# Kernel optimization log

Hardware: AMD Instinct MI355X
Metric: run time of the kernel (lower is better)

## Reference

```python
import jax, jax.numpy as jnp
import numpy as np

MODEL_DIM = 1024
NUM_HEADS = 16
HEAD_DIM = MODEL_DIM // NUM_HEADS
ROPE_THETA = 10000.0


def _rotate_half(x):
    x1, x2 = jnp.split(x, 2, axis=-1)
    return jnp.concatenate((-x2, x1), axis=-1)


def _rope_cos_sin(seq_len, dtype):
    inv_freq = 1.0 / (ROPE_THETA ** (jnp.arange(0, HEAD_DIM, 2, dtype=jnp.float32) / HEAD_DIM))
    pos = jnp.arange(seq_len, dtype=jnp.float32)
    freqs = jnp.einsum('i,j->ij', pos, inv_freq)  # [S, HEAD_DIM/2]
    emb = jnp.concatenate((freqs, freqs), axis=-1)  # [S, HEAD_DIM]
    return jnp.cos(emb).astype(dtype), jnp.sin(emb).astype(dtype)


def setup_inputs() -> dict:
    key = jax.random.key(0)
    ks = jax.random.split(key, 9)
    B, S, D = 4, 2048, MODEL_DIM
    scale = 1.0 / np.sqrt(D)
    inp = {
        'x': jax.random.normal(ks[0], (B, S, D), dtype=jnp.float32),
        'key_padding_mask': jnp.ones((B, S), dtype=bool),
        'wq': jax.random.normal(ks[1], (D, D), dtype=jnp.float32) * scale,
        'bq': jnp.zeros((D,), dtype=jnp.float32),
        'wk': jax.random.normal(ks[2], (D, D), dtype=jnp.float32) * scale,
        'bk': jnp.zeros((D,), dtype=jnp.float32),
        'wv': jax.random.normal(ks[3], (D, D), dtype=jnp.float32) * scale,
        'bv': jnp.zeros((D,), dtype=jnp.float32),
        'wo': jax.random.normal(ks[4], (D, D), dtype=jnp.float32) * scale,
        'bo': jnp.zeros((D,), dtype=jnp.float32),
    }
    return inp


def reference(x, key_padding_mask, wq, bq, wk, bk, wv, bv, wo, bo):
    B, S, D = x.shape
    H, Hd = NUM_HEADS, HEAD_DIM
    q = (x @ wq + bq).reshape(B, S, H, Hd).transpose(0, 2, 1, 3)
    k = (x @ wk + bk).reshape(B, S, H, Hd).transpose(0, 2, 1, 3)
    v = (x @ wv + bv).reshape(B, S, H, Hd).transpose(0, 2, 1, 3)
    cos, sin = _rope_cos_sin(S, x.dtype)  # [S, Hd]
    cos = cos[None, None]
    sin = sin[None, None]
    q = q * cos + _rotate_half(q) * sin
    k = k * cos + _rotate_half(k) * sin
    scores = jnp.einsum('bhqd,bhkd->bhqk', q, k) / jnp.sqrt(jnp.asarray(Hd, x.dtype))
    mask = key_padding_mask[:, None, None, :]
    scores = jnp.where(mask, scores, jnp.finfo(scores.dtype).min)
    attn = jax.nn.softmax(scores, axis=-1)
    ctx = jnp.einsum('bhqk,bhkd->bhqd', attn, v)
    ctx = ctx.transpose(0, 2, 1, 3).reshape(B, S, D)
    out = ctx @ wo + bo
    out = out * key_padding_mask[:, :, None].astype(out.dtype)
    return out
```

## Files before the change

### kernel.cpp

```cpp
#include <hip/hip_runtime.h>
#include <math.h>

#define S_LEN  2048
#define NH     16
#define HD     64
#define DMODEL 1024
#define BATCH  4
#define M_TOK  (BATCH * S_LEN)

typedef __bf16 bf16x8 __attribute__((ext_vector_type(8)));
typedef float  floatx4 __attribute__((ext_vector_type(4)));
typedef float  floatx16 __attribute__((ext_vector_type(16)));

typedef __attribute__((address_space(1))) const void cg_void;
typedef __attribute__((address_space(3))) void lds_void;

__device__ __forceinline__ void gload16(const void* g, void* l) {
    __builtin_amdgcn_global_load_lds((cg_void*)g, (lds_void*)l, 16, 0, 0);
}

__device__ __forceinline__ unsigned short f2bf(float f) {
    unsigned int u = __builtin_bit_cast(unsigned int, f);
    u = (u + 0x7FFF + ((u >> 16) & 1)) >> 16;
    return (unsigned short)u;
}

__device__ __forceinline__ unsigned cvtpk(float lo, float hi) {
    unsigned r;
    asm volatile("v_cvt_pk_bf16_f32 %0, %1, %2" : "=v"(r) : "v"(lo), "v"(hi));
    return r;
}

__device__ __forceinline__ void swap32(unsigned &a, unsigned &b) {
    asm volatile("v_permlane32_swap_b32 %0, %1" : "+v"(a), "+v"(b));
}

__global__ void rope_table_kernel(float* __restrict__ cs, float* __restrict__ sn) {
    int idx = blockIdx.x * 256 + threadIdx.x;
    int j = idx & 31;
    int s = idx >> 5;
    double invf = pow(10000.0, -(double)j / 32.0);
    double a = (double)s * invf;
    cs[idx] = (float)cos(a);
    sn[idx] = (float)sin(a);
}

__global__ void convert_x_kernel(const float* __restrict__ x, unsigned short* __restrict__ xb) {
    int idx = blockIdx.x * 256 + threadIdx.x;
    float4 a = *reinterpret_cast<const float4*>(&x[(size_t)idx * 4]);
    ushort4 o;
    o.x = f2bf(a.x); o.y = f2bf(a.y); o.z = f2bf(a.z); o.w = f2bf(a.w);
    *reinterpret_cast<ushort4*>(&xb[(size_t)idx * 4]) = o;
}

__global__ void convert_transpose_w(const float* __restrict__ w, unsigned short* __restrict__ wt) {
    __shared__ float tile[32][33];
    int tx  = threadIdx.x & 31;
    int ty8 = threadIdx.x >> 5;
    int n0 = blockIdx.x * 32;
    int k0 = blockIdx.y * 32;
    #pragma unroll
    for (int i = 0; i < 4; ++i)
        tile[ty8 + i * 8][tx] = w[(size_t)(k0 + ty8 + i * 8) * DMODEL + n0 + tx];
    __syncthreads();
    #pragma unroll
    for (int i = 0; i < 4; ++i)
        wt[(size_t)(n0 + ty8 + i * 8) * DMODEL + k0 + tx] = f2bf(tile[tx][ty8 + i * 8]);
}

__global__ __launch_bounds__(256)
void gemm_qkv(const unsigned short* __restrict__ A, const unsigned short* __restrict__ Bt,
              const float* __restrict__ bq, const float* __restrict__ bk,
              const float* __restrict__ bv,
              const float* __restrict__ cs, const float* __restrict__ sn,
              unsigned short* __restrict__ qbf, unsigned short* __restrict__ kbf,
              unsigned short* __restrict__ vtb)
{
    constexpr int K = DMODEL;
    __shared__ unsigned short As[2][128 * 32];
    __shared__ unsigned short Bs[2][128 * 32];

    const int tid  = threadIdx.x;
    const int lane = tid & 63;
    const int w    = tid >> 6;
    const int wm   = w >> 1;
    const int wn   = w & 1;
    const int row0 = blockIdx.y * 128;
    const int col0 = blockIdx.x * 128;

    const int sr  = lane >> 2;
    const int sk8 = (lane & 3) * 8;
    const int fr  = lane & 15;
    const int fk  = (lane >> 4) * 8;

    floatx4 acc[4][4] = {};

    #pragma unroll
    for (int t = 0; t < 2; ++t) {
        const int chunk = w * 32 + t * 16;
        gload16(A  + (size_t)(row0 + chunk + sr) * K + sk8, &As[0][chunk * 32]);
        gload16(Bt + (size_t)(col0 + chunk + sr) * K + sk8, &Bs[0][chunk * 32]);
    }

    for (int kt = 0; kt < K / 32; ++kt) {
        __syncthreads();
        if (kt + 1 < K / 32) {
            const int nb = (kt + 1) & 1;
            const int k0 = (kt + 1) * 32;
            #pragma unroll
            for (int t = 0; t < 2; ++t) {
                const int chunk = w * 32 + t * 16;
                gload16(A  + (size_t)(row0 + chunk + sr) * K + k0 + sk8, &As[nb][chunk * 32]);
                gload16(Bt + (size_t)(col0 + chunk + sr) * K + k0 + sk8, &Bs[nb][chunk * 32]);
            }
        }
        const int cur = kt & 1;
        bf16x8 av[4], bv4[4];
        #pragma unroll
        for (int m = 0; m < 4; ++m)
            av[m] = *reinterpret_cast<const bf16x8*>(&As[cur][(wm * 64 + m * 16 + fr) * 32 + fk]);
        #pragma unroll
        for (int n = 0; n < 4; ++n)
            bv4[n] = *reinterpret_cast<const bf16x8*>(&Bs[cur][(wn * 64 + n * 16 + fr) * 32 + fk]);
        #pragma unroll
        for (int m = 0; m < 4; ++m)
            #pragma unroll
            for (int n = 0; n < 4; ++n)
                acc[m][n] = __builtin_amdgcn_mfma_f32_16x16x32_bf16(av[m], bv4[n], acc[m][n], 0, 0, 0);
    }

    const int rbase = lane >> 4;
    const int sect  = col0 >> 10;
    const int c0    = col0 & 1023;

    if (sect == 2) {
        #pragma unroll
        for (int m = 0; m < 4; ++m)
            #pragma unroll
            for (int n = 0; n < 4; ++n) {
                const int c  = c0 + wn * 64 + n * 16 + fr;
                const int hh = c >> 6, d = c & 63;
                const int mr0 = row0 + wm * 64 + m * 16 + rbase * 4;
                const int bb = mr0 >> 11, ss = mr0 & (S_LEN - 1);
                const float bc = bv[c];
                ushort4 pk4;
                pk4.x = f2bf(acc[m][n][0] + bc);
                pk4.y = f2bf(acc[m][n][1] + bc);
                pk4.z = f2bf(acc[m][n][2] + bc);
                pk4.w = f2bf(acc[m][n][3] + bc);
                *reinterpret_cast<ushort4*>(
                    &vtb[((size_t)(bb * NH + hh) * HD + d) * S_LEN + ss]) = pk4;
            }
    } else {
        unsigned short* outp = sect ? kbf : qbf;
        const float* bias = sect ? bk : bq;
        const float sc = sect ? 1.0f : 0.125f;
        #pragma unroll
        for (int m = 0; m < 4; ++m)
            #pragma unroll
            for (int n = 0; n < 2; ++n) {
                const int c  = c0 + wn * 64 + n * 16 + fr;
                const int hh = c >> 6, d = c & 63;
                const float b1 = bias[c], b2 = bias[c + 32];
                #pragma unroll
                for (int r = 0; r < 4; ++r) {
                    const int mr = row0 + wm * 64 + m * 16 + rbase * 4 + r;
                    const int bb = mr >> 11, ss = mr & (S_LEN - 1);
                    const float v1 = acc[m][n][r] + b1;
                    const float v2 = acc[m][n + 2][r] + b2;
                    const float co = cs[ss * 32 + d];
                    const float si = sn[ss * 32 + d];
                    const size_t base = ((size_t)(bb * NH + hh) * S_LEN + ss) * HD + d;
                    outp[base]      = f2bf((v1 * co - v2 * si) * sc);
                    outp[base + 32] = f2bf((v2 * co + v1 * si) * sc);
                }
            }
    }
}

__global__ __launch_bounds__(256)
void attn_mfma2(const unsigned short* __restrict__ qbf,
                const unsigned short* __restrict__ kbf,
                const unsigned short* __restrict__ vtb,
                const int* __restrict__ mask,
                unsigned short* __restrict__ ctxb)
{
    __shared__ unsigned short Ks[2][64 * 64];
    __shared__ unsigned short Vs[2][64 * 64];
    __shared__ float biasP[2048];

    const int tid  = threadIdx.x;
    const int lane = tid & 63;
    const int w    = tid >> 6;
    const int bh   = blockIdx.x;
    const int b    = bh >> 4;
    const int h    = bh & 15;
    const int q0   = blockIdx.y * 128 + w * 32;
    const size_t hb = (size_t)bh * S_LEN * HD;
    const int* mrow_g = mask + b * S_LEN;

    const int lo5 = lane & 31;
    const int hi5 = lane >> 5;
    const int srow   = lane >> 3;
    const int schunk = (lane & 7) ^ srow;

    for (int i = tid; i < 2048; i += 256) {
        const int kt = i >> 6, rem = i & 63;
        const int hig = rem >> 5, kb = (rem >> 4) & 1, reg = rem & 15;
        const int key = kt * 64 + kb * 32 + hig * 4 + (reg & 3) + ((reg >> 2) << 3);
        biasP[i] = mrow_g[key] ? 0.0f : -3.0e38f;
    }

    bf16x8 qf[4];
    #pragma unroll
    for (int ks = 0; ks < 4; ++ks)
        qf[ks] = *reinterpret_cast<const bf16x8*>(
            &qbf[hb + (size_t)(q0 + lo5) * HD + ks * 16 + hi5 * 8]);

    floatx16 oacc[2];
    #pragma unroll
    for (int v = 0; v < 2; ++v)
        #pragma unroll
        for (int i = 0; i < 16; ++i) oacc[v][i] = 0.0f;
    float mrow = -3.0e38f, lrow = 0.0f;

    #define STAGE(KT, BUF)                                                                  \
        _Pragma("unroll")                                                                   \
        for (int t = 0; t < 2; ++t) {                                                       \
            const int r0 = w * 16 + t * 8;                                                  \
            gload16(kbf + hb + (size_t)((KT) * 64 + r0 + srow) * HD + schunk * 8,           \
                    &Ks[BUF][r0 * 64]);                                                     \
            gload16(vtb + ((size_t)bh * HD + r0 + srow) * S_LEN + (KT) * 64 + schunk * 8,   \
                    &Vs[BUF][r0 * 64]);                                                     \
        }

    STAGE(0, 0)

    for (int kt = 0; kt < S_LEN / 64; ++kt) {
        __syncthreads();
        if (kt + 1 < S_LEN / 64) { STAGE(kt + 1, (kt + 1) & 1) }
        const int cur = kt & 1;

        floatx16 sacc[2];
        #pragma unroll
        for (int kb = 0; kb < 2; ++kb) {
            const float4* bp = reinterpret_cast<const float4*>(&biasP[kt * 64 + hi5 * 32 + kb * 16]);
            #pragma unroll
            for (int t = 0; t < 4; ++t) {
                const float4 b4 = bp[t];
                sacc[kb][t * 4 + 0] = b4.x; sacc[kb][t * 4 + 1] = b4.y;
                sacc[kb][t * 4 + 2] = b4.z; sacc[kb][t * 4 + 3] = b4.w;
            }
        }

        __builtin_amdgcn_s_setprio(1);
        #pragma unroll
        for (int kb = 0; kb < 2; ++kb) {
            #pragma unroll
            for (int ks = 0; ks < 4; ++ks) {
                const bf16x8 ak = *reinterpret_cast<const bf16x8*>(
                    (const char*)&Ks[cur][0] + (kb * 32 + lo5) * 128 +
                    ((ks * 32 + hi5 * 16) ^ ((lo5 & 7) << 4)));
                sacc[kb] = __builtin_amdgcn_mfma_f32_32x32x16_bf16(ak, qf[ks], sacc[kb], 0, 0, 0);
            }
        }
        __builtin_amdgcn_s_setprio(0);

        float pmax = sacc[0][0];
        #pragma unroll
        for (int i = 1; i < 16; ++i) pmax = fmaxf(pmax, sacc[0][i]);
        #pragma unroll
        for (int i = 0; i < 16; ++i) pmax = fmaxf(pmax, sacc[1][i]);
        pmax = fmaxf(pmax, __shfl_xor(pmax, 32));
        const float mnew = fmaxf(mrow, pmax);
        const float fscale = __expf(mrow - mnew);
        mrow = mnew;
        float rs = 0.0f;
        #pragma unroll
        for (int kb = 0; kb < 2; ++kb)
            #pragma unroll
            for (int i = 0; i < 16; ++i) {
                const float p = __expf(sacc[kb][i] - mnew);
                sacc[kb][i] = p;
                rs += p;
            }
        rs += __shfl_xor(rs, 32);
        lrow = lrow * fscale + rs;
        #pragma unroll
        for (int v = 0; v < 2; ++v)
            #pragma unroll
            for (int i = 0; i < 16; ++i) oacc[v][i] *= fscale;

        unsigned U0[8], U1[8];
        #pragma unroll
        for (int kb = 0; kb < 2; ++kb)
            #pragma unroll
            for (int s = 0; s < 4; ++s) {
                U0[kb * 4 + s] = cvtpk(sacc[kb][4 * s + 0], sacc[kb][4 * s + 1]);
                U1[kb * 4 + s] = cvtpk(sacc[kb][4 * s + 2], sacc[kb][4 * s + 3]);
            }
        union PF { unsigned u[4]; bf16x8 v; };
        PF pf[4];
        #pragma unroll
        for (int ks = 0; ks < 4; ++ks) {
            unsigned a0 = U0[2 * ks], b0 = U0[2 * ks + 1];
            swap32(a0, b0);
            unsigned a1 = U1[2 * ks], b1 = U1[2 * ks + 1];
            swap32(a1, b1);
            pf[ks].u[0] = a0; pf[ks].u[1] = a1;
            pf[ks].u[2] = b0; pf[ks].u[3] = b1;
        }

        __builtin_amdgcn_s_setprio(1);
        #pragma unroll
        for (int vb = 0; vb < 2; ++vb) {
            #pragma unroll
            for (int ks = 0; ks < 4; ++ks) {
                const bf16x8 av = *reinterpret_cast<const bf16x8*>(
                    (const char*)&Vs[cur][0] + (vb * 32 + lo5) * 128 +
                    ((ks * 32 + hi5 * 16) ^ ((lo5 & 7) << 4)));
                oacc[vb] = __builtin_amdgcn_mfma_f32_32x32x16_bf16(av, pf[ks].v, oacc[vb], 0, 0, 0);
            }
        }
        __builtin_amdgcn_s_setprio(0);
    }

    const float inv = 1.0f / lrow;
    unsigned short* dst = &ctxb[((size_t)b * S_LEN + q0 + lo5) * DMODEL + h * HD];
    #pragma unroll
    for (int vb = 0; vb < 2; ++vb)
        #pragma unroll
        for (int s = 0; s < 4; ++s) {
            const int d0 = vb * 32 + s * 8 + hi5 * 4;
            ushort4 o4;
            o4.x = f2bf(oacc[vb][4 * s + 0] * inv);
            o4.y = f2bf(oacc[vb][4 * s + 1] * inv);
            o4.z = f2bf(oacc[vb][4 * s + 2] * inv);
            o4.w = f2bf(oacc[vb][4 * s + 3] * inv);
            *reinterpret_cast<ushort4*>(&dst[d0]) = o4;
        }
    #undef STAGE
}

__global__ __launch_bounds__(256)
void gemm_out(const unsigned short* __restrict__ A, const unsigned short* __restrict__ Bt,
              const float* __restrict__ bias, const int* __restrict__ mask,
              float* __restrict__ C)
{
    constexpr int K = DMODEL;
    __shared__ unsigned short As[2][128 * 32];
    __shared__ unsigned short Bs[2][128 * 32];

    const int tid  = threadIdx.x;
    const int lane = tid & 63;
    const int w    = tid >> 6;
    const int wm   = w >> 1;
    const int wn   = w & 1;
    const int row0 = blockIdx.y * 128;
    const int col0 = blockIdx.x * 128;

    const int sr  = lane >> 2;
    const int sk8 = (lane & 3) * 8;
    const int fr  = lane & 15;
    const int fk  = (lane >> 4) * 8;

    floatx4 acc[4][4] = {};

    #pragma unroll
    for (int t = 0; t < 2; ++t) {
        const int chunk = w * 32 + t * 16;
        gload16(A  + (size_t)(row0 + chunk + sr) * K + sk8, &As[0][chunk * 32]);
        gload16(Bt + (size_t)(col0 + chunk + sr) * K + sk8, &Bs[0][chunk * 32]);
    }

    for (int kt = 0; kt < K / 32; ++kt) {
        __syncthreads();
        if (kt + 1 < K / 32) {
            const int nb = (kt + 1) & 1;
            const int k0 = (kt + 1) * 32;
            #pragma unroll
            for (int t = 0; t < 2; ++t) {
                const int chunk = w * 32 + t * 16;
                gload16(A  + (size_t)(row0 + chunk + sr) * K + k0 + sk8, &As[nb][chunk * 32]);
                gload16(Bt + (size_t)(col0 + chunk + sr) * K + k0 + sk8, &Bs[nb][chunk * 32]);
            }
        }
        const int cur = kt & 1;
        bf16x8 av[4], bv4[4];
        #pragma unroll
        for (int m = 0; m < 4; ++m)
            av[m] = *reinterpret_cast<const bf16x8*>(&As[cur][(wm * 64 + m * 16 + fr) * 32 + fk]);
        #pragma unroll
        for (int n = 0; n < 4; ++n)
            bv4[n] = *reinterpret_cast<const bf16x8*>(&Bs[cur][(wn * 64 + n * 16 + fr) * 32 + fk]);
        #pragma unroll
        for (int m = 0; m < 4; ++m)
            #pragma unroll
            for (int n = 0; n < 4; ++n)
                acc[m][n] = __builtin_amdgcn_mfma_f32_16x16x32_bf16(av[m], bv4[n], acc[m][n], 0, 0, 0);
    }

    const int rbase = lane >> 4;
    #pragma unroll
    for (int m = 0; m < 4; ++m)
        #pragma unroll
        for (int n = 0; n < 4; ++n) {
            const int c = col0 + wn * 64 + n * 16 + fr;
            const float bc = bias[c];
            #pragma unroll
            for (int r = 0; r < 4; ++r) {
                const int mr = row0 + wm * 64 + m * 16 + rbase * 4 + r;
                C[(size_t)mr * DMODEL + c] = mask[mr] ? (acc[m][n][r] + bc) : 0.0f;
            }
        }
}

extern "C" void kernel_launch(void* const* d_in, const int* in_sizes, int n_in,
                              void* d_out, int out_size, void* d_ws, size_t ws_size,
                              hipStream_t stream) {
    const float* x    = (const float*)d_in[0];
    const int*   mask = (const int*)d_in[1];
    const float* wq = (const float*)d_in[2];
    const float* bq = (const float*)d_in[3];
    const float* wk = (const float*)d_in[4];
    const float* bk = (const float*)d_in[5];
    const float* wv = (const float*)d_in[6];
    const float* bv = (const float*)d_in[7];
    const float* wo = (const float*)d_in[8];
    const float* bo = (const float*)d_in[9];
    float* out = (float*)d_out;

    const size_t QKV = (size_t)M_TOK * DMODEL;
    const size_t WSZ = (size_t)DMODEL * DMODEL;
    unsigned short* xb     = (unsigned short*)d_ws;
    unsigned short* wstack = xb + QKV;
    unsigned short* wto    = wstack + 3 * WSZ;
    unsigned short* qbf    = wto + WSZ;
    unsigned short* kbf    = qbf + QKV;
    unsigned short* vtb    = kbf + QKV;
    unsigned short* ctxb   = vtb + QKV;
    float* cs = (float*)(ctxb + QKV);
    float* sn = cs + (size_t)S_LEN * 32;

    rope_table_kernel<<<S_LEN * 32 / 256, 256, 0, stream>>>(cs, sn);
    convert_x_kernel<<<QKV / (256 * 4), 256, 0, stream>>>(x, xb);

    dim3 tgrid(DMODEL / 32, DMODEL / 32);
    convert_transpose_w<<<tgrid, 256, 0, stream>>>(wq, wstack);
    convert_transpose_w<<<tgrid, 256, 0, stream>>>(wk, wstack + WSZ);
    convert_transpose_w<<<tgrid, 256, 0, stream>>>(wv, wstack + 2 * WSZ);
    convert_transpose_w<<<tgrid, 256, 0, stream>>>(wo, wto);

    dim3 qkvgrid(3 * DMODEL / 128, M_TOK / 128);
    gemm_qkv<<<qkvgrid, 256, 0, stream>>>(xb, wstack, bq, bk, bv, cs, sn, qbf, kbf, vtb);

    dim3 agrid(BATCH * NH, S_LEN / 128);
    attn_mfma2<<<agrid, 256, 0, stream>>>(qbf, kbf, vtb, mask, ctxb);

    dim3 ogrid(DMODEL / 128, M_TOK / 128);
    gemm_out<<<ogrid, 256, 0, stream>>>(ctxb, wto, bo, mask, out);
}
```

Before: 354.6 us.

## Fuse prep kernels, precompute mask bias, use exp2 softmax with lazy rescale, swizzle GEMM blocks

Merges the rope-table, x-conversion and four weight-transpose launches into one prep kernel, which also builds a global mask-bias table plus per-tile all-valid flags so attention skips the per-block bias construction and the bias loads for fully unmasked tiles. Softmax now uses exp2 with log2e folded into the Q scale, a max3-based reduction tree, split partial sums, and a lazy rescale that only updates the running max when it grows by more than a threshold. Both GEMMs remap block indices in an XCD-aware interleave to improve cache locality. The lazy-rescale threshold trades some numeric headroom for fewer rescales, and the gemm_out remap assumes the grid width is 8.

Measured after the change: 341.5 us. -3.7%, faster.

```diff
diff --git a/kernel.cpp b/kernel.cpp
--- a/kernel.cpp
+++ b/kernel.cpp
@@ -15,6 +15,12 @@
 typedef __attribute__((address_space(1))) const void cg_void;
 typedef __attribute__((address_space(3))) void lds_void;
 
+#if __has_builtin(__builtin_amdgcn_exp2f)
+#define EXP2(x) __builtin_amdgcn_exp2f(x)
+#else
+#define EXP2(x) exp2f(x)
+#endif
+
 __device__ __forceinline__ void gload16(const void* g, void* l) {
     __builtin_amdgcn_global_load_lds((cg_void*)g, (lds_void*)l, 16, 0, 0);
 }
@@ -35,37 +41,73 @@
     asm volatile("v_permlane32_swap_b32 %0, %1" : "+v"(a), "+v"(b));
 }
 
-__global__ void rope_table_kernel(float* __restrict__ cs, float* __restrict__ sn) {
-    int idx = blockIdx.x * 256 + threadIdx.x;
-    int j = idx & 31;
-    int s = idx >> 5;
-    double invf = pow(10000.0, -(double)j / 32.0);
-    double a = (double)s * invf;
-    cs[idx] = (float)cos(a);
-    sn[idx] = (float)sin(a);
-}
-
-__global__ void convert_x_kernel(const float* __restrict__ x, unsigned short* __restrict__ xb) {
-    int idx = blockIdx.x * 256 + threadIdx.x;
-    float4 a = *reinterpret_cast<const float4*>(&x[(size_t)idx * 4]);
-    ushort4 o;
-    o.x = f2bf(a.x); o.y = f2bf(a.y); o.z = f2bf(a.z); o.w = f2bf(a.w);
-    *reinterpret_cast<ushort4*>(&xb[(size_t)idx * 4]) = o;
-}
-
-__global__ void convert_transpose_w(const float* __restrict__ w, unsigned short* __restrict__ wt) {
+__device__ __forceinline__ float max3f(float a, float b, float c) {
+    float r;
+    asm("v_max3_f32 %0, %1, %2, %3" : "=v"(r) : "v"(a), "v"(b), "v"(c));
+    return r;
+}
+
+__global__ __launch_bounds__(256)
+void prep_kernel(const float* __restrict__ x,
+                 const float* __restrict__ wq, const float* __restrict__ wk,
+                 const float* __restrict__ wv, const float* __restrict__ wo,
+                 const int* __restrict__ mask,
+                 unsigned short* __restrict__ xb, unsigned short* __restrict__ wstack,
+                 unsigned short* __restrict__ wto,
+                 float* __restrict__ cs, float* __restrict__ sn,
+                 float* __restrict__ biasG, int* __restrict__ flags)
+{
     __shared__ float tile[32][33];
-    int tx  = threadIdx.x & 31;
-    int ty8 = threadIdx.x >> 5;
-    int n0 = blockIdx.x * 32;
-    int k0 = blockIdx.y * 32;
-    #pragma unroll
-    for (int i = 0; i < 4; ++i)
-        tile[ty8 + i * 8][tx] = w[(size_t)(k0 + ty8 + i * 8) * DMODEL + n0 + tx];
-    __syncthreads();
-    #pragma unroll
-    for (int i = 0; i < 4; ++i)
-        wt[(size_t)(n0 + ty8 + i * 8) * DMODEL + k0 + tx] = f2bf(tile[tx][ty8 + i * 8]);
+    const int blk = blockIdx.x;
+    const int tid = threadIdx.x;
+    constexpr size_t WSZ = (size_t)DMODEL * DMODEL;
+
+    if (blk < 8192) {
+        const int idx = blk * 256 + tid;
+        float4 a = *reinterpret_cast<const float4*>(&x[(size_t)idx * 4]);
+        ushort4 o;
+        o.x = f2bf(a.x); o.y = f2bf(a.y); o.z = f2bf(a.z); o.w = f2bf(a.w);
+        *reinterpret_cast<ushort4*>(&xb[(size_t)idx * 4]) = o;
+    } else if (blk < 12288) {
+        const int rel = blk - 8192;
+        const int mat = rel >> 10;
+        const float* w = (mat == 0) ? wq : (mat == 1) ? wk : (mat == 2) ? wv : wo;
+        unsigned short* wt = (mat < 3) ? (wstack + (size_t)mat * WSZ) : wto;
+        const int rel10 = rel & 1023;
+        const int n0 = (rel10 & 31) * 32;
+        const int k0 = (rel10 >> 5) * 32;
+        const int tx  = tid & 31;
+        const int ty8 = tid >> 5;
+        #pragma unroll
+        for (int i = 0; i < 4; ++i)
+            tile[ty8 + i * 8][tx] = w[(size_t)(k0 + ty8 + i * 8) * DMODEL + n0 + tx];
+        __syncthreads();
+        #pragma unroll
+        for (int i = 0; i < 4; ++i)
+            wt[(size_t)(n0 + ty8 + i * 8) * DMODEL + k0 + tx] = f2bf(tile[tx][ty8 + i * 8]);
+    } else if (blk < 12544) {
+        const int idx = (blk - 12288) * 256 + tid;
+        const int j = idx & 31;
+        const int s = idx >> 5;
+        double invf = pow(10000.0, -(double)j / 32.0);
+        double a = (double)s * invf;
+        cs[idx] = (float)cos(a);
+        sn[idx] = (float)sin(a);
+    } else {
+        for (int i = tid; i < BATCH * S_LEN; i += 256) {
+            const int b = i >> 11, r = i & 2047;
+            const int kt = r >> 6, rem = r & 63;
+            const int hig = rem >> 5, kbb = (rem >> 4) & 1, reg = rem & 15;
+            const int key = kt * 64 + kbb * 32 + hig * 4 + (reg & 3) + ((reg >> 2) << 3);
+            biasG[i] = mask[b * S_LEN + key] ? 0.0f : -3.0e38f;
+        }
+        for (int i = tid; i < BATCH * 32; i += 256) {
+            const int b = i >> 5, kt = i & 31;
+            int ok = 1;
+            for (int j = 0; j < 64; ++j) ok &= (mask[b * S_LEN + kt * 64 + j] != 0);
+            flags[i] = ok;
+        }
+    }
 }
 
 __global__ __launch_bounds__(256)
@@ -85,8 +127,15 @@
     const int w    = tid >> 6;
     const int wm   = w >> 1;
     const int wn   = w & 1;
-    const int row0 = blockIdx.y * 128;
-    const int col0 = blockIdx.x * 128;
+
+    {
+    }
+    const int gx   = gridDim.x;
+    int lin = blockIdx.y * gx + blockIdx.x;
+    const int cpx = (gx * gridDim.y) >> 3;
+    lin = (lin & 7) * cpx + (lin >> 3);
+    const int row0 = (lin / gx) * 128;
+    const int col0 = (lin % gx) * 128;
 
     const int sr  = lane >> 2;
     const int sk8 = (lane & 3) * 8;
@@ -154,7 +203,7 @@
     } else {
         unsigned short* outp = sect ? kbf : qbf;
         const float* bias = sect ? bk : bq;
-        const float sc = sect ? 1.0f : 0.125f;
+        const float sc = sect ? 1.0f : 0.125f * 1.44269504088896f;
         #pragma unroll
         for (int m = 0; m < 4; ++m)
             #pragma unroll
@@ -182,12 +231,12 @@
 void attn_mfma2(const unsigned short* __restrict__ qbf,
                 const unsigned short* __restrict__ kbf,
                 const unsigned short* __restrict__ vtb,
-                const int* __restrict__ mask,
+                const float* __restrict__ biasG,
+                const int* __restrict__ flags,
                 unsigned short* __restrict__ ctxb)
 {
     __shared__ unsigned short Ks[2][64 * 64];
     __shared__ unsigned short Vs[2][64 * 64];
-    __shared__ float biasP[2048];
 
     const int tid  = threadIdx.x;
     const int lane = tid & 63;
@@ -197,19 +246,11 @@
     const int h    = bh & 15;
     const int q0   = blockIdx.y * 128 + w * 32;
     const size_t hb = (size_t)bh * S_LEN * HD;
-    const int* mrow_g = mask + b * S_LEN;
 
     const int lo5 = lane & 31;
     const int hi5 = lane >> 5;
     const int srow   = lane >> 3;
     const int schunk = (lane & 7) ^ srow;
-
-    for (int i = tid; i < 2048; i += 256) {
-        const int kt = i >> 6, rem = i & 63;
-        const int hig = rem >> 5, kb = (rem >> 4) & 1, reg = rem & 15;
-        const int key = kt * 64 + kb * 32 + hig * 4 + (reg & 3) + ((reg >> 2) << 3);
-        biasP[i] = mrow_g[key] ? 0.0f : -3.0e38f;
-    }
 
     bf16x8 qf[4];
     #pragma unroll
@@ -242,15 +283,22 @@
         const int cur = kt & 1;
 
         floatx16 sacc[2];
-        #pragma unroll
-        for (int kb = 0; kb < 2; ++kb) {
-            const float4* bp = reinterpret_cast<const float4*>(&biasP[kt * 64 + hi5 * 32 + kb * 16]);
-            #pragma unroll
-            for (int t = 0; t < 4; ++t) {
-                const float4 b4 = bp[t];
-                sacc[kb][t * 4 + 0] = b4.x; sacc[kb][t * 4 + 1] = b4.y;
-                sacc[kb][t * 4 + 2] = b4.z; sacc[kb][t * 4 + 3] = b4.w;
-            }
+        if (flags[b * 32 + kt]) {
+            #pragma unroll
+            for (int kb = 0; kb < 2; ++kb)
+                #pragma unroll
+                for (int i = 0; i < 16; ++i) sacc[kb][i] = 0.0f;
+        } else {
+            const float4* bp = reinterpret_cast<const float4*>(
+                &biasG[(size_t)(b * 32 + kt) * 64 + hi5 * 32]);
+            #pragma unroll
+            for (int kb = 0; kb < 2; ++kb)
+                #pragma unroll
+                for (int t = 0; t < 4; ++t) {
+                    const float4 b4 = bp[kb * 4 + t];
+                    sacc[kb][t * 4 + 0] = b4.x; sacc[kb][t * 4 + 1] = b4.y;
+                    sacc[kb][t * 4 + 2] = b4.z; sacc[kb][t * 4 + 3] = b4.w;
+                }
         }
 
         __builtin_amdgcn_s_setprio(1);
@@ -266,30 +314,50 @@
         }
         __builtin_amdgcn_s_setprio(0);
 
-        float pmax = sacc[0][0];
-        #pragma unroll
-        for (int i = 1; i < 16; ++i) pmax = fmaxf(pmax, sacc[0][i]);
-        #pragma unroll
-        for (int i = 0; i < 16; ++i) pmax = fmaxf(pmax, sacc[1][i]);
+        float r0 = max3f(sacc[0][0],  sacc[0][1],  sacc[0][2]);
+        float r1 = max3f(sacc[0][3],  sacc[0][4],  sacc[0][5]);
+        float r2 = max3f(sacc[0][6],  sacc[0][7],  sacc[0][8]);
+        float r3 = max3f(sacc[0][9],  sacc[0][10], sacc[0][11]);
+        float r4 = max3f(sacc[0][12], sacc[0][13], sacc[0][14]);
+        float r5 = max3f(sacc[1][0],  sacc[1][1],  sacc[1][2]);
+        float r6 = max3f(sacc[1][3],  sacc[1][4],  sacc[1][5]);
+        float r7 = max3f(sacc[1][6],  sacc[1][7],  sacc[1][8]);
+        float r8 = max3f(sacc[1][9],  sacc[1][10], sacc[1][11]);
+        float r9 = max3f(sacc[1][12], sacc[1][13], sacc[1][14]);
+        float s1 = max3f(r0, r1, r2);
+        float s2 = max3f(r3, r4, r5);
+        float s3 = max3f(r6, r7, r8);
+        float s4 = max3f(r9, sacc[0][15], sacc[1][15]);
+        float pmax = fmaxf(max3f(s1, s2, s3), s4);
         pmax = fmaxf(pmax, __shfl_xor(pmax, 32));
-        const float mnew = fmaxf(mrow, pmax);
-        const float fscale = __expf(mrow - mnew);
-        mrow = mnew;
-        float rs = 0.0f;
+
+        if (!__all(pmax <= mrow + 8.0f)) {
+            const float mnew = fmaxf(mrow, pmax);
+            const float fscale = EXP2(mrow - mnew);
+            mrow = mnew;
+            lrow *= fscale;
+            #pragma unroll
+            for (int v = 0; v < 2; ++v)
+                #pragma unroll
+                for (int i = 0; i < 16; ++i) oacc[v][i] *= fscale;
+        }
+
+        float rs0 = 0.0f, rs1 = 0.0f, rs2 = 0.0f, rs3 = 0.0f;
         #pragma unroll
         for (int kb = 0; kb < 2; ++kb)
             #pragma unroll
-            for (int i = 0; i < 16; ++i) {
-                const float p = __expf(sacc[kb][i] - mnew);
-                sacc[kb][i] = p;
-                rs += p;
-            }
+            for (int i = 0; i < 16; i += 4) {
+                float p0 = EXP2(sacc[kb][i + 0] - mrow);
+                float p1 = EXP2(sacc[kb][i + 1] - mrow);
+                float p2 = EXP2(sacc[kb][i + 2] - mrow);
+                float p3 = EXP2(sacc[kb][i + 3] - mrow);
+                sacc[kb][i + 0] = p0; sacc[kb][i + 1] = p1;
+                sacc[kb][i + 2] = p2; sacc[kb][i + 3] = p3;
+                rs0 += p0; rs1 += p1; rs2 += p2; rs3 += p3;
+            }
+        float rs = (rs0 + rs1) + (rs2 + rs3);
         rs += __shfl_xor(rs, 32);
-        lrow = lrow * fscale + rs;
-        #pragma unroll
-        for (int v = 0; v < 2; ++v)
-            #pragma unroll
-            for (int i = 0; i < 16; ++i) oacc[v][i] *= fscale;
+        lrow += rs;
 
         unsigned U0[8], U1[8];
         #pragma unroll
@@ -356,8 +424,13 @@
     const int w    = tid >> 6;
     const int wm   = w >> 1;
     const int wn   = w & 1;
-    const int row0 = blockIdx.y * 128;
-    const int col0 = blockIdx.x * 128;
+
+    const int gx   = gridDim.x;
+    int lin = blockIdx.y * gx + blockIdx.x;
+    const int cpx = (gx * gridDim.y) >> 3;
+    lin = (lin & 7) * cpx + (lin >> 3);
+    const int row0 = (lin >> 3) * 128;
+    const int col0 = (lin & 7) * 128;
 
     const int sr  = lane >> 2;
     const int sk8 = (lane & 3) * 8;
@@ -439,23 +512,19 @@
     unsigned short* kbf    = qbf + QKV;
     unsigned short* vtb    = kbf + QKV;
     unsigned short* ctxb   = vtb + QKV;
-    float* cs = (float*)(ctxb + QKV);
-    float* sn = cs + (size_t)S_LEN * 32;
-
-    rope_table_kernel<<<S_LEN * 32 / 256, 256, 0, stream>>>(cs, sn);
-    convert_x_kernel<<<QKV / (256 * 4), 256, 0, stream>>>(x, xb);
-
-    dim3 tgrid(DMODEL / 32, DMODEL / 32);
-    convert_transpose_w<<<tgrid, 256, 0, stream>>>(wq, wstack);
-    convert_transpose_w<<<tgrid, 256, 0, stream>>>(wk, wstack + WSZ);
-    convert_transpose_w<<<tgrid, 256, 0, stream>>>(wv, wstack + 2 * WSZ);
-    convert_transpose_w<<<tgrid, 256, 0, stream>>>(wo, wto);
+    float* cs    = (float*)(ctxb + QKV);
+    float* sn    = cs + (size_t)S_LEN * 32;
+    float* biasG = sn + (size_t)S_LEN * 32;
+    int*   flags = (int*)(biasG + (size_t)BATCH * S_LEN);
+
+    prep_kernel<<<12545, 256, 0, stream>>>(x, wq, wk, wv, wo, mask,
+                                           xb, wstack, wto, cs, sn, biasG, flags);
 
     dim3 qkvgrid(3 * DMODEL / 128, M_TOK / 128);
     gemm_qkv<<<qkvgrid, 256, 0, stream>>>(xb, wstack, bq, bk, bv, cs, sn, qbf, kbf, vtb);
 
     dim3 agrid(BATCH * NH, S_LEN / 128);
-    attn_mfma2<<<agrid, 256, 0, stream>>>(qbf, kbf, vtb, mask, ctxb);
+    attn_mfma2<<<agrid, 256, 0, stream>>>(qbf, kbf, vtb, biasG, flags, ctxb);
 
     dim3 ogrid(DMODEL / 128, M_TOK / 128);
     gemm_out<<<ogrid, 256, 0, stream>>>(ctxb, wto, bo, mask, out);
```
